# Kernel tuning notes

Measured on AMD Instinct MI355X. Metric: run time of the kernel, lower is better.

The kernel has to match this reference:

```python
import jax, jax.numpy as jnp
import numpy as np

D = 128
N = 768
EPS = 1e-5

def _layernorm(x, w, b):
    m = jnp.mean(x, axis=-1, keepdims=True)
    v = jnp.mean(jnp.square(x - m), axis=-1, keepdims=True)
    return (x - m) * jax.lax.rsqrt(v + EPS) * w + b

def _linear(x, w, b):
    # torch Linear convention: w is [out, in]
    return jnp.einsum('...i,oi->...o', x, w) + b

def setup_inputs() -> dict:
    key = jax.random.key(0)
    ks = jax.random.split(key, 8)
    s = 1.0 / np.sqrt(D)
    d = {
        'pair': jax.random.normal(ks[0], (N, N, D), dtype=jnp.float32),
        'ln_in_w': jnp.ones((D,), jnp.float32), 'ln_in_b': jnp.zeros((D,), jnp.float32),
        'lp_w': jax.random.uniform(ks[1], (D, D), jnp.float32, -s, s), 'lp_b': jnp.zeros((D,), jnp.float32),
        'lg_w': jax.random.uniform(ks[2], (D, D), jnp.float32, -s, s), 'lg_b': jnp.zeros((D,), jnp.float32),
        'rp_w': jax.random.uniform(ks[3], (D, D), jnp.float32, -s, s), 'rp_b': jnp.zeros((D,), jnp.float32),
        'rg_w': jax.random.uniform(ks[4], (D, D), jnp.float32, -s, s), 'rg_b': jnp.zeros((D,), jnp.float32),
        'cn_w': jnp.ones((D,), jnp.float32), 'cn_b': jnp.zeros((D,), jnp.float32),
        'op_w': jax.random.uniform(ks[5], (D, D), jnp.float32, -s, s), 'op_b': jnp.zeros((D,), jnp.float32),
        'og_w': jax.random.uniform(ks[6], (D, D), jnp.float32, -s, s), 'og_b': jnp.zeros((D,), jnp.float32),
        'ln_out_w': jnp.ones((D,), jnp.float32), 'ln_out_b': jnp.zeros((D,), jnp.float32),
    }
    return d

def reference(pair, ln_in_w, ln_in_b, lp_w, lp_b, lg_w, lg_b, rp_w, rp_b, rg_w, rg_b,
              cn_w, cn_b, op_w, op_b, og_w, og_b, ln_out_w, ln_out_b):
    z = _layernorm(pair, ln_in_w, ln_in_b)
    left = jax.nn.sigmoid(_linear(z, lg_w, lg_b)) * _linear(z, lp_w, lp_b)
    right = jax.nn.sigmoid(_linear(z, rg_w, rg_b)) * _linear(z, rp_w, rp_b)
    # outgoing direction: pair(i,j) = sum_k left(i,k,d) * right(j,k,d)
    tri = jnp.einsum('ikd,jkd->ijd', left, right)
    tri = _layernorm(tri, cn_w, cn_b)
    tri = jax.nn.sigmoid(_linear(pair, og_w, og_b)) * _linear(tri, op_w, op_b)
    return _layernorm(pair + tri, ln_out_w, ln_out_b)
```

## Files before the change

kernel.cpp:

```cpp
#include <hip/hip_runtime.h>

#define N 768
#define D 128
#define NSQ (N*N)
#define EPS 1e-5f

typedef __bf16 bf16;
typedef __bf16 bf16x4 __attribute__((ext_vector_type(4)));
typedef __bf16 bf16x8 __attribute__((ext_vector_type(8)));
typedef float f32x4 __attribute__((ext_vector_type(4)));

__device__ __forceinline__ void gld16(const void* g, void* l) {
    __builtin_amdgcn_global_load_lds(
        (const __attribute__((address_space(1))) unsigned int*)g,
        (__attribute__((address_space(3))) unsigned int*)l, 16, 0, 0);
}

__device__ __forceinline__ void barrier_lds() {
    asm volatile("s_waitcnt lgkmcnt(0)" ::: "memory");
    __builtin_amdgcn_s_barrier();
    __builtin_amdgcn_sched_barrier(0);
}

__global__ void k_convert_w(const float* __restrict__ lp, const float* __restrict__ lg,
                            const float* __restrict__ rp, const float* __restrict__ rg,
                            const float* __restrict__ op, const float* __restrict__ og,
                            bf16* __restrict__ dst) {
    const float* srcs[6] = {lp, lg, rp, rg, op, og};
    int m = blockIdx.y;
    int i = blockIdx.x * 256 + threadIdx.x;
    dst[m * 16384 + i] = (bf16)srcs[m][i];
}

__global__ __launch_bounds__(512, 2) void k_ln_gate2(
    const float* __restrict__ pair, const float* __restrict__ lnw, const float* __restrict__ lnb,
    const bf16* __restrict__ wbf,
    const float* __restrict__ lp_b, const float* __restrict__ lg_b,
    const float* __restrict__ rp_b, const float* __restrict__ rg_b,
    bf16* __restrict__ left_t, bf16* __restrict__ right_t)
{
    __shared__ bf16 zt[2][64 * 128];

    const int t = threadIdx.x;
    const int lane = t & 63, wid = t >> 6;
    const int side = wid >> 2, dq = wid & 3;
    const int lr = lane & 15, lh = lane >> 4;

    const bf16* wPsrc = wbf + (side ? 2 : 0) * 16384;
    const bf16* wGsrc = wbf + (side ? 3 : 1) * 16384;
    const float* bPp = side ? rp_b : lp_b;
    const float* bGp = side ? rg_b : lg_b;
    bf16* dst = side ? right_t : left_t;

    bf16x8 aP[4][2], aG[4][2];
    #pragma unroll
    for (int kk = 0; kk < 4; ++kk)
        #pragma unroll
        for (int m = 0; m < 2; ++m) {
            int rd = dq * 32 + m * 16 + lr;
            aP[kk][m] = *(const bf16x8*)(wPsrc + rd * 128 + (kk * 4 + lh) * 8);
            aG[kk][m] = *(const bf16x8*)(wGsrc + rd * 128 + (kk * 4 + lh) * 8);
        }
    float bP[2], bG[2];
    #pragma unroll
    for (int m = 0; m < 2; ++m) {
        bP[m] = bPp[dq * 32 + m * 16 + lr];
        bG[m] = bGp[dq * 32 + m * 16 + lr];
    }

    const int r8 = t >> 3, q = t & 7;

    f32x4 lw0 = *(const f32x4*)(lnw + q * 16);
    f32x4 lw1 = *(const f32x4*)(lnw + q * 16 + 4);
    f32x4 lw2 = *(const f32x4*)(lnw + q * 16 + 8);
    f32x4 lw3 = *(const f32x4*)(lnw + q * 16 + 12);
    f32x4 lb0 = *(const f32x4*)(lnb + q * 16);
    f32x4 lb1 = *(const f32x4*)(lnb + q * 16 + 4);
    f32x4 lb2 = *(const f32x4*)(lnb + q * 16 + 8);
    f32x4 lb3 = *(const f32x4*)(lnb + q * 16 + 12);

    const int bid = blockIdx.x, gstride = gridDim.x;
    const int NT = NSQ / 64;

    f32x4 p0, p1, p2, p3;

    auto ln_to = [&](int b) {
        float x[16];
        #pragma unroll
        for (int e = 0; e < 4; ++e) {
            x[e] = p0[e]; x[4 + e] = p1[e]; x[8 + e] = p2[e]; x[12 + e] = p3[e];
        }
        float s1 = 0.f, s2 = 0.f;
        #pragma unroll
        for (int j = 0; j < 16; ++j) { s1 += x[j]; s2 += x[j] * x[j]; }
        s1 += __shfl_xor(s1, 1); s2 += __shfl_xor(s2, 1);
        s1 += __shfl_xor(s1, 2); s2 += __shfl_xor(s2, 2);
        s1 += __shfl_xor(s1, 4); s2 += __shfl_xor(s2, 4);
        float mean = s1 * (1.f / 128.f);
        float rstd = rsqrtf(s2 * (1.f / 128.f) - mean * mean + EPS);
        bf16x8 pk0, pk1;
        #pragma unroll
        for (int e = 0; e < 4; ++e) {
            pk0[e]     = (bf16)((x[e]      - mean) * rstd * lw0[e] + lb0[e]);
            pk0[4 + e] = (bf16)((x[4 + e]  - mean) * rstd * lw1[e] + lb1[e]);
            pk1[e]     = (bf16)((x[8 + e]  - mean) * rstd * lw2[e] + lb2[e]);
            pk1[4 + e] = (bf16)((x[12 + e] - mean) * rstd * lw3[e] + lb3[e]);
        }
        char* zb = (char*)&zt[b][0];
        *(bf16x8*)(zb + r8 * 256 + ((q * 2)     ^ (r8 & 7)) * 16) = pk0;
        *(bf16x8*)(zb + r8 * 256 + ((q * 2 + 1) ^ (r8 & 7)) * 16) = pk1;
    };
    auto load_regs = [&](int tile) {
        const float* prow = pair + (size_t)(tile * 64 + r8) * 128 + q * 16;
        p0 = *(const f32x4*)(prow);
        p1 = *(const f32x4*)(prow + 4);
        p2 = *(const f32x4*)(prow + 8);
        p3 = *(const f32x4*)(prow + 12);
    };

    load_regs(bid);
    ln_to(0);
    if (bid + gstride < NT) load_regs(bid + gstride);
    barrier_lds();

    int buf = 0;
    for (int tile = bid; tile < NT; tile += gstride) {
        const int row0 = tile * 64;
        const int nt = tile + gstride;

        if (nt < NT) ln_to(buf ^ 1);
        if (nt + gstride < NT) load_regs(nt + gstride);

        f32x4 accP[2][4] = {};
        f32x4 accG[2][4] = {};
        const char* zb = (const char*)&zt[buf][0];
        #pragma unroll
        for (int kk = 0; kk < 4; ++kk) {
            bf16x8 bz[4];
            #pragma unroll
            for (int n = 0; n < 4; ++n) {
                int rz = n * 16 + lr;
                bz[n] = *(const bf16x8*)(zb + rz * 256 + (((kk * 4 + lh)) ^ (rz & 7)) * 16);
            }
            #pragma unroll
            for (int m = 0; m < 2; ++m)
                #pragma unroll
                for (int n = 0; n < 4; ++n) {
                    accP[m][n] = __builtin_amdgcn_mfma_f32_16x16x32_bf16(bz[n], aP[kk][m], accP[m][n], 0, 0, 0);
                    accG[m][n] = __builtin_amdgcn_mfma_f32_16x16x32_bf16(bz[n], aG[kk][m], accG[m][n], 0, 0, 0);
                }
        }

        #pragma unroll
        for (int m = 0; m < 2; ++m) {
            const int d = dq * 32 + m * 16 + lr;
            bf16* drow = dst + (size_t)d * NSQ + row0 + lh * 4;
            #pragma unroll
            for (int n = 0; n < 4; ++n) {
                bf16x4 pk;
                #pragma unroll
                for (int reg = 0; reg < 4; ++reg) {
                    float g = accG[m][n][reg] + bG[m];
                    float p = accP[m][n][reg] + bP[m];
                    pk[reg] = (bf16)(p * (1.f / (1.f + __expf(-g))));
                }
                *(bf16x4*)(drow + n * 16) = pk;
            }
        }
        barrier_lds();
        buf ^= 1;
    }
}

__global__ __launch_bounds__(512, 2) void k_tri(
    const bf16* __restrict__ left_t, const bf16* __restrict__ right_t, bf16* __restrict__ tri_t)
{
    __shared__ bf16 at[2][256 * 64];
    __shared__ bf16 bt[2][256 * 64];
    const int t = threadIdx.x;
    const int b = blockIdx.x;
    const int xcd = b & 7;
    const int s = b >> 3;
    const int d = xcd * 16 + s / 9;
    const int tile = s % 9;
    const int ti = tile / 3, tj = tile % 3;
    const bf16* A = left_t + (size_t)d * NSQ;
    const bf16* B = right_t + (size_t)d * NSQ;
    const int i0 = ti * 256, j0 = tj * 256;

    const int lane = t & 63, wid = t >> 6;
    const int wr = wid >> 2, wc = wid & 3;
    const int lr = lane & 15, lh = lane >> 4;

    const bf16* SRC = (wid < 4) ? A : B;
    const int srcbase = (wid < 4) ? i0 : j0;
    const int w4 = wid & 3;
    auto stage4 = [&](int bf, int kt, int half) {
        char* dstb = (wid < 4) ? (char*)at[bf] : (char*)bt[bf];
        #pragma unroll
        for (int i2 = 0; i2 < 4; ++i2) {
            int i = half * 4 + i2;
            int rl = w4 * 64 + i * 8 + (lane >> 3);
            int lc = (lane & 7) ^ (rl & 7);
            gld16(SRC + (size_t)(srcbase + rl) * 768 + kt * 64 + lc * 8,
                  dstb + rl * 128 + (lane & 7) * 16);
        }
    };

    f32x4 acc[8][4] = {};

    stage4(0, 0, 0);
    stage4(0, 0, 1);
    asm volatile("s_waitcnt vmcnt(0)" ::: "memory");
    __builtin_amdgcn_s_barrier();
    __builtin_amdgcn_sched_barrier(0);

    for (int kt = 0; kt < 12; ++kt) {
        const int bf = kt & 1;
        const char* ab = (const char*)at[bf];
        const char* bb = (const char*)bt[bf];
        bf16x8 bff[4];
        #pragma unroll
        for (int kk = 0; kk < 2; ++kk) {
            #pragma unroll
            for (int mh = 0; mh < 2; ++mh) {
                const int ph = kk * 2 + mh;
                bf16x8 af[4];
                if (ph == 0) {
                    if (kt < 11) {
                        stage4(bf ^ 1, kt + 1, 0);
                        asm volatile("s_waitcnt vmcnt(4)" ::: "memory");
                    } else {
                        asm volatile("s_waitcnt vmcnt(0)" ::: "memory");
                    }
                    __builtin_amdgcn_s_barrier();
                    __builtin_amdgcn_sched_barrier(0);
                    #pragma unroll
                    for (int n = 0; n < 4; ++n) {
                        int r = wc * 64 + n * 16 + lr;
                        bff[n] = *(const bf16x8*)(bb + r * 128 + (((kk * 4 + lh)) ^ (r & 7)) * 16);
                    }
                    #pragma unroll
                    for (int mi = 0; mi < 4; ++mi) {
                        int r = wr * 128 + (mh * 4 + mi) * 16 + lr;
                        af[mi] = *(const bf16x8*)(ab + r * 128 + (((kk * 4 + lh)) ^ (r & 7)) * 16);
                    }
                    asm volatile("s_waitcnt lgkmcnt(0)" ::: "memory");
                    __builtin_amdgcn_sched_barrier(0);
                } else {
                    if (mh == 0) {
                        #pragma unroll
                        for (int n = 0; n < 4; ++n) {
                            int r = wc * 64 + n * 16 + lr;
                            bff[n] = *(const bf16x8*)(bb + r * 128 + (((kk * 4 + lh)) ^ (r & 7)) * 16);
                        }
                    }
                    #pragma unroll
                    for (int mi = 0; mi < 4; ++mi) {
                        int r = wr * 128 + (mh * 4 + mi) * 16 + lr;
                        af[mi] = *(const bf16x8*)(ab + r * 128 + (((kk * 4 + lh)) ^ (r & 7)) * 16);
                    }
                    if (ph == 1 && kt < 11) stage4(bf ^ 1, kt + 1, 1);
                    __builtin_amdgcn_s_barrier();
                    asm volatile("s_waitcnt lgkmcnt(0)" ::: "memory");
                    __builtin_amdgcn_sched_barrier(0);
                }
                __builtin_amdgcn_s_setprio(1);
                #pragma unroll
                for (int mi = 0; mi < 4; ++mi)
                    #pragma unroll
                    for (int n = 0; n < 4; ++n)
                        acc[mh * 4 + mi][n] = __builtin_amdgcn_mfma_f32_16x16x32_bf16(
                            bff[n], af[mi], acc[mh * 4 + mi][n], 0, 0, 0);
                __builtin_amdgcn_s_setprio(0);
                __builtin_amdgcn_s_barrier();
                __builtin_amdgcn_sched_barrier(0);
            }
        }
    }

    bf16* C = tri_t + (size_t)d * NSQ;
    #pragma unroll
    for (int m = 0; m < 8; ++m) {
        const int ri = i0 + wr * 128 + m * 16 + lr;
        bf16* crow = C + (size_t)ri * 768 + j0 + wc * 64 + lh * 4;
        #pragma unroll
        for (int n = 0; n < 4; ++n) {
            bf16x4 pk;
            #pragma unroll
            for (int reg = 0; reg < 4; ++reg)
                pk[reg] = (bf16)acc[m][n][reg];
            *(bf16x4*)(crow + n * 16) = pk;
        }
    }
}

__global__ __launch_bounds__(256, 2) void k_cln(
    const bf16* __restrict__ tri_t, const float* __restrict__ cnw, const float* __restrict__ cnb,
    bf16* __restrict__ tri_ln)
{
    __shared__ bf16 tile[256 * 128];
    __shared__ float mrs[256][2];
    const int t = threadIdx.x;
    const size_t ij = (size_t)blockIdx.x * 256 + t;
    float s1 = 0.f, s2 = 0.f;
    for (int dc = 0; dc < 16; ++dc) {
        bf16x8 pk;
        #pragma unroll
        for (int e = 0; e < 8; ++e) {
            int dd = dc * 8 + e;
            bf16 raw = tri_t[(size_t)dd * NSQ + ij];
            float v = (float)raw;
            s1 += v; s2 += v * v;
            pk[e] = raw;
        }
        *(bf16x8*)((char*)tile + t * 256 + (dc ^ (t & 7)) * 16) = pk;
    }
    float mean = s1 * (1.f / 128.f);
    float rstd = rsqrtf(s2 * (1.f / 128.f) - mean * mean + EPS);
    mrs[t][0] = mean; mrs[t][1] = rstd;
    __syncthreads();
    const size_t ij0 = (size_t)blockIdx.x * 256;
    #pragma unroll
    for (int c = 0; c < 16; ++c) {
        int sl = c * 256 + t;
        int rl = sl >> 4, cp = sl & 15, cl = cp ^ (rl & 7);
        bf16x8 raw = *(const bf16x8*)((const char*)tile + rl * 256 + cp * 16);
        float m = mrs[rl][0], r = mrs[rl][1];
        f32x4 w0 = *(const f32x4*)(cnw + cl * 8);
        f32x4 w1 = *(const f32x4*)(cnw + cl * 8 + 4);
        f32x4 b0 = *(const f32x4*)(cnb + cl * 8);
        f32x4 b1 = *(const f32x4*)(cnb + cl * 8 + 4);
        bf16x8 o;
        #pragma unroll
        for (int e = 0; e < 4; ++e) {
            o[e]     = (bf16)(((float)raw[e]     - m) * r * w0[e] + b0[e]);
            o[4 + e] = (bf16)(((float)raw[4 + e] - m) * r * w1[e] + b1[e]);
        }
        *(bf16x8*)(tri_ln + (ij0 + rl) * 128 + cl * 8) = o;
    }
}

__global__ __launch_bounds__(512, 2) void k_final2(
    const float* __restrict__ pair, const bf16* __restrict__ tri_ln,
    const bf16* __restrict__ wbf,
    const float* __restrict__ op_b, const float* __restrict__ og_b,
    const float* __restrict__ lnow, const float* __restrict__ lnob,
    float* __restrict__ out)
{
    __shared__ bf16 zt[64 * 128];
    __shared__ bf16 tt[2][64 * 128];
    __shared__ bf16 ub[64 * 136];

    const int t = threadIdx.x;
    const int lane = t & 63, wid = t >> 6;
    const int dq = wid & 3, wh = wid >> 2;
    const int lr = lane & 15, lh = lane >> 4;

    const bf16* opsrc = wbf + 4 * 16384;
    const bf16* ogsrc = wbf + 5 * 16384;

    bf16x8 aOG[4][2], aOP[4][2];
    #pragma unroll
    for (int kk = 0; kk < 4; ++kk)
        #pragma unroll
        for (int m = 0; m < 2; ++m) {
            int rd = dq * 32 + m * 16 + lr;
            aOG[kk][m] = *(const bf16x8*)(ogsrc + rd * 128 + (kk * 4 + lh) * 8);
            aOP[kk][m] = *(const bf16x8*)(opsrc + rd * 128 + (kk * 4 + lh) * 8);
        }
    f32x4 vbOG[2], vbOP[2];
    #pragma unroll
    for (int m = 0; m < 2; ++m) {
        vbOG[m] = *(const f32x4*)(og_b + dq * 32 + m * 16 + lh * 4);
        vbOP[m] = *(const f32x4*)(op_b + dq * 32 + m * 16 + lh * 4);
    }

    const int r8 = t >> 3, q = t & 7;
    f32x4 lw0 = *(const f32x4*)(lnow + q * 16);
    f32x4 lw1 = *(const f32x4*)(lnow + q * 16 + 4);
    f32x4 lw2 = *(const f32x4*)(lnow + q * 16 + 8);
    f32x4 lw3 = *(const f32x4*)(lnow + q * 16 + 12);
    f32x4 lb0 = *(const f32x4*)(lnob + q * 16);
    f32x4 lb1 = *(const f32x4*)(lnob + q * 16 + 4);
    f32x4 lb2 = *(const f32x4*)(lnob + q * 16 + 8);
    f32x4 lb3 = *(const f32x4*)(lnob + q * 16 + 12);

    const int bid = blockIdx.x, gstride = gridDim.x;

    auto stage_tt = [&](int buf, int tile) {
        const int row0 = tile * 64;
        #pragma unroll
        for (int c = 0; c < 2; ++c) {
            int s = c * 512 + t;
            int r = s >> 4, cp = s & 15, cl = cp ^ (r & 7);
            gld16(tri_ln + (size_t)(row0 + r) * 128 + cl * 8, (char*)tt[buf] + s * 16);
        }
    };

    stage_tt(0, bid);
    f32x4 pA0, pA1, pA2, pA3;
    {
        const float* prow = pair + (size_t)(bid * 64 + r8) * 128 + q * 16;
        pA0 = *(const f32x4*)(prow);
        pA1 = *(const f32x4*)(prow + 4);
        pA2 = *(const f32x4*)(prow + 8);
        pA3 = *(const f32x4*)(prow + 12);
    }

    int buf = 0;
    for (int tile = bid; tile < NSQ / 64; tile += gstride) {
        const int row0 = tile * 64;

        {
            bf16x8 pk0, pk1;
            #pragma unroll
            for (int e = 0; e < 4; ++e) {
                pk0[e]     = (bf16)pA0[e];
                pk0[4 + e] = (bf16)pA1[e];
                pk1[e]     = (bf16)pA2[e];
                pk1[4 + e] = (bf16)pA3[e];
            }
            char* zb = (char*)zt;
            *(bf16x8*)(zb + r8 * 256 + ((q * 2)     ^ (r8 & 7)) * 16) = pk0;
            *(bf16x8*)(zb + r8 * 256 + ((q * 2 + 1) ^ (r8 & 7)) * 16) = pk1;
        }
        barrier_lds();

        const int nt = tile + gstride;
        if (nt < NSQ / 64) stage_tt(buf ^ 1, nt);

        f32x4 pB0 = pA0, pB1 = pA1, pB2 = pA2, pB3 = pA3;
        if (nt < NSQ / 64) {
            const float* prow = pair + (size_t)(nt * 64 + r8) * 128 + q * 16;
            pB0 = *(const f32x4*)(prow);
            pB1 = *(const f32x4*)(prow + 4);
            pB2 = *(const f32x4*)(prow + 8);
            pB3 = *(const f32x4*)(prow + 12);
        }

        f32x4 accOG[2][2] = {};
        f32x4 accOP[2][2] = {};
        const char* zb = (const char*)zt;
        const char* tb = (const char*)tt[buf];
        #pragma unroll
        for (int kk = 0; kk < 4; ++kk) {
            bf16x8 bzp[2], bzt[2];
            #pragma unroll
            for (int n = 0; n < 2; ++n) {
                int rz = wh * 32 + n * 16 + lr;
                int phys = (kk * 4 + lh) ^ (rz & 7);
                bzp[n] = *(const bf16x8*)(zb + rz * 256 + phys * 16);
                bzt[n] = *(const bf16x8*)(tb + rz * 256 + phys * 16);
            }
            #pragma unroll
            for (int m = 0; m < 2; ++m)
                #pragma unroll
                for (int n = 0; n < 2; ++n) {
                    accOG[m][n] = __builtin_amdgcn_mfma_f32_16x16x32_bf16(aOG[kk][m], bzp[n], accOG[m][n], 0, 0, 0);
                    accOP[m][n] = __builtin_amdgcn_mfma_f32_16x16x32_bf16(aOP[kk][m], bzt[n], accOP[m][n], 0, 0, 0);
                }
        }

        #pragma unroll
        for (int m = 0; m < 2; ++m)
            #pragma unroll
            for (int n = 0; n < 2; ++n) {
                int rr = wh * 32 + n * 16 + lr;
                bf16x4 v;
                #pragma unroll
                for (int reg = 0; reg < 4; ++reg) {
                    float g = accOG[m][n][reg] + vbOG[m][reg];
                    float p = accOP[m][n][reg] + vbOP[m][reg];
                    v[reg] = (bf16)(p * (1.f / (1.f + __expf(-g))));
                }
                *(bf16x4*)(ub + rr * 136 + dq * 32 + m * 16 + lh * 4) = v;
            }
        barrier_lds();

        {
            float x[16];
            const bf16* ur = ub + r8 * 136 + q * 16;
            bf16x8 u0 = *(const bf16x8*)(ur);
            bf16x8 u1 = *(const bf16x8*)(ur + 8);
            #pragma unroll
            for (int e = 0; e < 4; ++e) {
                x[e]      = pA0[e] + (float)u0[e];
                x[4 + e]  = pA1[e] + (float)u0[4 + e];
                x[8 + e]  = pA2[e] + (float)u1[e];
                x[12 + e] = pA3[e] + (float)u1[4 + e];
            }
            float s1 = 0.f, s2 = 0.f;
            #pragma unroll
            for (int j = 0; j < 16; ++j) { s1 += x[j]; s2 += x[j] * x[j]; }
            s1 += __shfl_xor(s1, 1); s2 += __shfl_xor(s2, 1);
            s1 += __shfl_xor(s1, 2); s2 += __shfl_xor(s2, 2);
            s1 += __shfl_xor(s1, 4); s2 += __shfl_xor(s2, 4);
            float mean = s1 * (1.f / 128.f);
            float rstd = rsqrtf(s2 * (1.f / 128.f) - mean * mean + EPS);
            float* orow = out + (size_t)(row0 + r8) * 128 + q * 16;
            f32x4 o0, o1, o2, o3;
            #pragma unroll
            for (int e = 0; e < 4; ++e) {
                o0[e] = (x[e]      - mean) * rstd * lw0[e] + lb0[e];
                o1[e] = (x[4 + e]  - mean) * rstd * lw1[e] + lb1[e];
                o2[e] = (x[8 + e]  - mean) * rstd * lw2[e] + lb2[e];
                o3[e] = (x[12 + e] - mean) * rstd * lw3[e] + lb3[e];
            }
            *(f32x4*)(orow)      = o0;
            *(f32x4*)(orow + 4)  = o1;
            *(f32x4*)(orow + 8)  = o2;
            *(f32x4*)(orow + 12) = o3;
        }

        pA0 = pB0; pA1 = pB1; pA2 = pB2; pA3 = pB3;
        buf ^= 1;
    }
}

extern "C" void kernel_launch(void* const* d_in, const int* in_sizes, int n_in,
                              void* d_out, int out_size, void* d_ws, size_t ws_size,
                              hipStream_t stream) {
    const float* pair    = (const float*)d_in[0];
    const float* ln_in_w = (const float*)d_in[1];
    const float* ln_in_b = (const float*)d_in[2];
    const float* lp_w    = (const float*)d_in[3];
    const float* lp_b    = (const float*)d_in[4];
    const float* lg_w    = (const float*)d_in[5];
    const float* lg_b    = (const float*)d_in[6];
    const float* rp_w    = (const float*)d_in[7];
    const float* rp_b    = (const float*)d_in[8];
    const float* rg_w    = (const float*)d_in[9];
    const float* rg_b    = (const float*)d_in[10];
    const float* cn_w    = (const float*)d_in[11];
    const float* cn_b    = (const float*)d_in[12];
    const float* op_w    = (const float*)d_in[13];
    const float* op_b    = (const float*)d_in[14];
    const float* og_w    = (const float*)d_in[15];
    const float* og_b    = (const float*)d_in[16];
    const float* ln_out_w = (const float*)d_in[17];
    const float* ln_out_b = (const float*)d_in[18];

    const size_t HALF = (size_t)128 * NSQ * 2;
    char* ws = (char*)d_ws;
    bf16* wbf     = (bf16*)ws;
    bf16* right_t = (bf16*)(ws + 196608);
    bf16* tri_ln  = right_t;
    bf16* left_t  = (bf16*)d_out;
    bf16* tri_t   = (bf16*)((char*)d_out + HALF);

    k_convert_w<<<dim3(64, 6), 256, 0, stream>>>(lp_w, lg_w, rp_w, rg_w, op_w, og_w, wbf);
    k_ln_gate2<<<dim3(512), 512, 0, stream>>>(pair, ln_in_w, ln_in_b, wbf,
                                              lp_b, lg_b, rp_b, rg_b, left_t, right_t);
    k_tri<<<dim3(1152), 512, 0, stream>>>(left_t, right_t, tri_t);
    k_cln<<<dim3(NSQ / 256), 256, 0, stream>>>(tri_t, cn_w, cn_b, tri_ln);
    k_final2<<<dim3(512), 512, 0, stream>>>(pair, tri_ln, wbf, op_b, og_b,
                                            ln_out_w, ln_out_b, (float*)d_out);
}
```

Before: 545.5 us.

## Fold layernorm affine into projection weights and restructure tri GEMM inner loop

The layernorm scale is folded into the bf16 projection weights and the layernorm shift into precomputed biases by a new small kernel. This removes the per-element affine work and parameter loads from the input-LN and the tri-LN kernels. Separately, the tri GEMM main loop is restructured to load all eight A fragments per k-step and issue 32 MFMAs together, with fewer barriers per iteration. That raises register pressure and adds an extra kernel launch. Rounding changes slightly because the scale is now applied before bf16 conversion of the weights.

```diff
diff --git a/kernel.cpp b/kernel.cpp
--- a/kernel.cpp
+++ b/kernel.cpp
@@ -25,18 +25,39 @@
 __global__ void k_convert_w(const float* __restrict__ lp, const float* __restrict__ lg,
                             const float* __restrict__ rp, const float* __restrict__ rg,
                             const float* __restrict__ op, const float* __restrict__ og,
+                            const float* __restrict__ lnw, const float* __restrict__ cnw,
                             bf16* __restrict__ dst) {
     const float* srcs[6] = {lp, lg, rp, rg, op, og};
     int m = blockIdx.y;
     int i = blockIdx.x * 256 + threadIdx.x;
-    dst[m * 16384 + i] = (bf16)srcs[m][i];
+    float v = srcs[m][i];
+    int k = i & 127;
+    if (m < 4) v *= lnw[k];
+    else if (m == 4) v *= cnw[k];
+    dst[m * 16384 + i] = (bf16)v;
+}
+
+__global__ void k_bias(const float* __restrict__ lp_w, const float* __restrict__ lg_w,
+                       const float* __restrict__ rp_w, const float* __restrict__ rg_w,
+                       const float* __restrict__ op_w,
+                       const float* __restrict__ lp_b, const float* __restrict__ lg_b,
+                       const float* __restrict__ rp_b, const float* __restrict__ rg_b,
+                       const float* __restrict__ op_b,
+                       const float* __restrict__ lnb, const float* __restrict__ cnb,
+                       float* __restrict__ outb) {
+    int m = blockIdx.x;
+    int d = threadIdx.x;
+    const float* W[5] = {lp_w, lg_w, rp_w, rg_w, op_w};
+    const float* B[5] = {lp_b, lg_b, rp_b, rg_b, op_b};
+    const float* beta = (m < 4) ? lnb : cnb;
+    float s = B[m][d];
+    for (int k = 0; k < 128; ++k) s += W[m][d * 128 + k] * beta[k];
+    outb[m * 128 + d] = s;
 }
 
 __global__ __launch_bounds__(512, 2) void k_ln_gate2(
-    const float* __restrict__ pair, const float* __restrict__ lnw, const float* __restrict__ lnb,
-    const bf16* __restrict__ wbf,
-    const float* __restrict__ lp_b, const float* __restrict__ lg_b,
-    const float* __restrict__ rp_b, const float* __restrict__ rg_b,
+    const float* __restrict__ pair, const bf16* __restrict__ wbf,
+    const float* __restrict__ badj,
     bf16* __restrict__ left_t, bf16* __restrict__ right_t)
 {
     __shared__ bf16 zt[2][64 * 128];
@@ -48,8 +69,8 @@
 
     const bf16* wPsrc = wbf + (side ? 2 : 0) * 16384;
     const bf16* wGsrc = wbf + (side ? 3 : 1) * 16384;
-    const float* bPp = side ? rp_b : lp_b;
-    const float* bGp = side ? rg_b : lg_b;
+    const float* bPp = badj + (side ? 2 : 0) * 128;
+    const float* bGp = badj + (side ? 3 : 1) * 128;
     bf16* dst = side ? right_t : left_t;
 
     bf16x8 aP[4][2], aG[4][2];
@@ -69,15 +90,6 @@
     }
 
     const int r8 = t >> 3, q = t & 7;
-
-    f32x4 lw0 = *(const f32x4*)(lnw + q * 16);
-    f32x4 lw1 = *(const f32x4*)(lnw + q * 16 + 4);
-    f32x4 lw2 = *(const f32x4*)(lnw + q * 16 + 8);
-    f32x4 lw3 = *(const f32x4*)(lnw + q * 16 + 12);
-    f32x4 lb0 = *(const f32x4*)(lnb + q * 16);
-    f32x4 lb1 = *(const f32x4*)(lnb + q * 16 + 4);
-    f32x4 lb2 = *(const f32x4*)(lnb + q * 16 + 8);
-    f32x4 lb3 = *(const f32x4*)(lnb + q * 16 + 12);
 
     const int bid = blockIdx.x, gstride = gridDim.x;
     const int NT = NSQ / 64;
@@ -101,10 +113,10 @@
         bf16x8 pk0, pk1;
         #pragma unroll
         for (int e = 0; e < 4; ++e) {
-            pk0[e]     = (bf16)((x[e]      - mean) * rstd * lw0[e] + lb0[e]);
-            pk0[4 + e] = (bf16)((x[4 + e]  - mean) * rstd * lw1[e] + lb1[e]);
-            pk1[e]     = (bf16)((x[8 + e]  - mean) * rstd * lw2[e] + lb2[e]);
-            pk1[4 + e] = (bf16)((x[12 + e] - mean) * rstd * lw3[e] + lb3[e]);
+            pk0[e]     = (bf16)((x[e]      - mean) * rstd);
+            pk0[4 + e] = (bf16)((x[4 + e]  - mean) * rstd);
+            pk1[e]     = (bf16)((x[8 + e]  - mean) * rstd);
+            pk1[4 + e] = (bf16)((x[12 + e] - mean) * rstd);
         }
         char* zb = (char*)&zt[b][0];
         *(bf16x8*)(zb + r8 * 256 + ((q * 2)     ^ (r8 & 7)) * 16) = pk0;
@@ -219,64 +231,44 @@
         const int bf = kt & 1;
         const char* ab = (const char*)at[bf];
         const char* bb = (const char*)bt[bf];
-        bf16x8 bff[4];
         #pragma unroll
         for (int kk = 0; kk < 2; ++kk) {
-            #pragma unroll
-            for (int mh = 0; mh < 2; ++mh) {
-                const int ph = kk * 2 + mh;
-                bf16x8 af[4];
-                if (ph == 0) {
-                    if (kt < 11) {
-                        stage4(bf ^ 1, kt + 1, 0);
-                        asm volatile("s_waitcnt vmcnt(4)" ::: "memory");
-                    } else {
-                        asm volatile("s_waitcnt vmcnt(0)" ::: "memory");
-                    }
-                    __builtin_amdgcn_s_barrier();
-                    __builtin_amdgcn_sched_barrier(0);
-                    #pragma unroll
-                    for (int n = 0; n < 4; ++n) {
-                        int r = wc * 64 + n * 16 + lr;
-                        bff[n] = *(const bf16x8*)(bb + r * 128 + (((kk * 4 + lh)) ^ (r & 7)) * 16);
-                    }
-                    #pragma unroll
-                    for (int mi = 0; mi < 4; ++mi) {
-                        int r = wr * 128 + (mh * 4 + mi) * 16 + lr;
-                        af[mi] = *(const bf16x8*)(ab + r * 128 + (((kk * 4 + lh)) ^ (r & 7)) * 16);
-                    }
-                    asm volatile("s_waitcnt lgkmcnt(0)" ::: "memory");
-                    __builtin_amdgcn_sched_barrier(0);
+            if (kk == 0) {
+                if (kt < 11) {
+                    stage4(bf ^ 1, kt + 1, 0);
+                    asm volatile("s_waitcnt vmcnt(4)" ::: "memory");
                 } else {
-                    if (mh == 0) {
-                        #pragma unroll
-                        for (int n = 0; n < 4; ++n) {
-                            int r = wc * 64 + n * 16 + lr;
-                            bff[n] = *(const bf16x8*)(bb + r * 128 + (((kk * 4 + lh)) ^ (r & 7)) * 16);
-                        }
-                    }
-                    #pragma unroll
-                    for (int mi = 0; mi < 4; ++mi) {
-                        int r = wr * 128 + (mh * 4 + mi) * 16 + lr;
-                        af[mi] = *(const bf16x8*)(ab + r * 128 + (((kk * 4 + lh)) ^ (r & 7)) * 16);
-                    }
-                    if (ph == 1 && kt < 11) stage4(bf ^ 1, kt + 1, 1);
-                    __builtin_amdgcn_s_barrier();
-                    asm volatile("s_waitcnt lgkmcnt(0)" ::: "memory");
-                    __builtin_amdgcn_sched_barrier(0);
+                    asm volatile("s_waitcnt vmcnt(0)" ::: "memory");
                 }
-                __builtin_amdgcn_s_setprio(1);
-                #pragma unroll
-                for (int mi = 0; mi < 4; ++mi)
-                    #pragma unroll
-                    for (int n = 0; n < 4; ++n)
-                        acc[mh * 4 + mi][n] = __builtin_amdgcn_mfma_f32_16x16x32_bf16(
-                            bff[n], af[mi], acc[mh * 4 + mi][n], 0, 0, 0);
-                __builtin_amdgcn_s_setprio(0);
                 __builtin_amdgcn_s_barrier();
                 __builtin_amdgcn_sched_barrier(0);
-            }
-        }
+            } else {
+                if (kt < 11) stage4(bf ^ 1, kt + 1, 1);
+            }
+            bf16x8 bff[4], af[8];
+            #pragma unroll
+            for (int n = 0; n < 4; ++n) {
+                int r = wc * 64 + n * 16 + lr;
+                bff[n] = *(const bf16x8*)(bb + r * 128 + (((kk * 4 + lh)) ^ (r & 7)) * 16);
+            }
+            #pragma unroll
+            for (int mi = 0; mi < 8; ++mi) {
+                int r = wr * 128 + mi * 16 + lr;
+                af[mi] = *(const bf16x8*)(ab + r * 128 + (((kk * 4 + lh)) ^ (r & 7)) * 16);
+            }
+            asm volatile("s_waitcnt lgkmcnt(0)" ::: "memory");
+            __builtin_amdgcn_sched_barrier(0);
+            __builtin_amdgcn_s_setprio(1);
+            #pragma unroll
+            for (int mi = 0; mi < 8; ++mi)
+                #pragma unroll
+                for (int n = 0; n < 4; ++n)
+                    acc[mi][n] = __builtin_amdgcn_mfma_f32_16x16x32_bf16(
+                        bff[n], af[mi], acc[mi][n], 0, 0, 0);
+            __builtin_amdgcn_s_setprio(0);
+        }
+        __builtin_amdgcn_s_barrier();
+        __builtin_amdgcn_sched_barrier(0);
     }
 
     bf16* C = tri_t + (size_t)d * NSQ;
@@ -296,8 +288,7 @@
 }
 
 __global__ __launch_bounds__(256, 2) void k_cln(
-    const bf16* __restrict__ tri_t, const float* __restrict__ cnw, const float* __restrict__ cnb,
-    bf16* __restrict__ tri_ln)
+    const bf16* __restrict__ tri_t, bf16* __restrict__ tri_ln)
 {
     __shared__ bf16 tile[256 * 128];
     __shared__ float mrs[256][2];
@@ -327,16 +318,10 @@
         int rl = sl >> 4, cp = sl & 15, cl = cp ^ (rl & 7);
         bf16x8 raw = *(const bf16x8*)((const char*)tile + rl * 256 + cp * 16);
         float m = mrs[rl][0], r = mrs[rl][1];
-        f32x4 w0 = *(const f32x4*)(cnw + cl * 8);
-        f32x4 w1 = *(const f32x4*)(cnw + cl * 8 + 4);
-        f32x4 b0 = *(const f32x4*)(cnb + cl * 8);
-        f32x4 b1 = *(const f32x4*)(cnb + cl * 8 + 4);
         bf16x8 o;
         #pragma unroll
-        for (int e = 0; e < 4; ++e) {
-            o[e]     = (bf16)(((float)raw[e]     - m) * r * w0[e] + b0[e]);
-            o[4 + e] = (bf16)(((float)raw[4 + e] - m) * r * w1[e] + b1[e]);
-        }
+        for (int e = 0; e < 8; ++e)
+            o[e] = (bf16)(((float)raw[e] - m) * r);
         *(bf16x8*)(tri_ln + (ij0 + rl) * 128 + cl * 8) = o;
     }
 }
@@ -344,7 +329,7 @@
 __global__ __launch_bounds__(512, 2) void k_final2(
     const float* __restrict__ pair, const bf16* __restrict__ tri_ln,
     const bf16* __restrict__ wbf,
-    const float* __restrict__ op_b, const float* __restrict__ og_b,
+    const float* __restrict__ opb_adj, const float* __restrict__ og_b,
     const float* __restrict__ lnow, const float* __restrict__ lnob,
     float* __restrict__ out)
 {
@@ -373,7 +358,7 @@
     #pragma unroll
     for (int m = 0; m < 2; ++m) {
         vbOG[m] = *(const f32x4*)(og_b + dq * 32 + m * 16 + lh * 4);
-        vbOP[m] = *(const f32x4*)(op_b + dq * 32 + m * 16 + lh * 4);
+        vbOP[m] = *(const f32x4*)(opb_adj + dq * 32 + m * 16 + lh * 4);
     }
 
     const int r8 = t >> 3, q = t & 7;
@@ -543,17 +528,21 @@
 
     const size_t HALF = (size_t)128 * NSQ * 2;
     char* ws = (char*)d_ws;
-    bf16* wbf     = (bf16*)ws;
-    bf16* right_t = (bf16*)(ws + 196608);
-    bf16* tri_ln  = right_t;
-    bf16* left_t  = (bf16*)d_out;
-    bf16* tri_t   = (bf16*)((char*)d_out + HALF);
-
-    k_convert_w<<<dim3(64, 6), 256, 0, stream>>>(lp_w, lg_w, rp_w, rg_w, op_w, og_w, wbf);
-    k_ln_gate2<<<dim3(512), 512, 0, stream>>>(pair, ln_in_w, ln_in_b, wbf,
-                                              lp_b, lg_b, rp_b, rg_b, left_t, right_t);
+    bf16*  wbf     = (bf16*)ws;
+    float* badj    = (float*)(ws + 196608);
+    bf16*  right_t = (bf16*)(ws + 196608 + 4096);
+    bf16*  tri_ln  = right_t;
+    bf16*  left_t  = (bf16*)d_out;
+    bf16*  tri_t   = (bf16*)((char*)d_out + HALF);
+
+    k_convert_w<<<dim3(64, 6), 256, 0, stream>>>(lp_w, lg_w, rp_w, rg_w, op_w, og_w,
+                                                 ln_in_w, cn_w, wbf);
+    k_bias<<<dim3(5), 128, 0, stream>>>(lp_w, lg_w, rp_w, rg_w, op_w,
+                                        lp_b, lg_b, rp_b, rg_b, op_b,
+                                        ln_in_b, cn_b, badj);
+    k_ln_gate2<<<dim3(512), 512, 0, stream>>>(pair, wbf, badj, left_t, right_t);
     k_tri<<<dim3(1152), 512, 0, stream>>>(left_t, right_t, tri_t);
-    k_cln<<<dim3(NSQ / 256), 256, 0, stream>>>(tri_t, cn_w, cn_b, tri_ln);
-    k_final2<<<dim3(512), 512, 0, stream>>>(pair, tri_ln, wbf, op_b, og_b,
+    k_cln<<<dim3(NSQ / 256), 256, 0, stream>>>(tri_t, tri_ln);
+    k_final2<<<dim3(512), 512, 0, stream>>>(pair, tri_ln, wbf, badj + 512, og_b,
                                             ln_out_w, ln_out_b, (float*)d_out);
 }
```

After: 538.8 us. Within noise of the previous version (-1.2%).
